# Optimization experiments

Hardware: AMD Instinct MI355X
Metric: run time of the kernel (lower is better)

The kernel has to match this reference:

```python
import jax, jax.numpy as jnp
import numpy as np

GRID_SIZE = 5
SPLINE_ORDER = 3
KH, KW = 3, 3
STRIDE, PAD, DIL = 1, 1, 1


def make_grid(in_features, dtype=jnp.float32):
    # uniform grid over [-1, 1], extended by spline_order on each side
    h = 2.0 / GRID_SIZE
    g = jnp.arange(-SPLINE_ORDER, GRID_SIZE + SPLINE_ORDER + 1, dtype=dtype) * h - 1.0
    return jnp.broadcast_to(g, (in_features, g.shape[0]))  # (in, G)


def b_splines(x, grid):
    # x: (N, in); grid: (in, G). Cox-de Boor recursion.
    xg = x[..., None]  # (N, in, 1)
    bases = ((xg >= grid[:, :-1]) & (xg < grid[:, 1:])).astype(x.dtype)  # (N, in, G-1)
    for k in range(1, SPLINE_ORDER + 1):
        left = (xg - grid[:, : -(k + 1)]) / (grid[:, k:-1] - grid[:, : -(k + 1)])
        right = (grid[:, k + 1:] - xg) / (grid[:, k + 1:] - grid[:, 1:-k])
        bases = left * bases[..., :-1] + right * bases[..., 1:]
    return bases  # (N, in, grid_size + spline_order)


def setup_inputs() -> dict:
    key = jax.random.key(0)
    k1, k2, k3, k4 = jax.random.split(key, 4)
    B, C, H, W = 4, 64, 64, 64
    out_ch = 128
    patch_dim = C * KH * KW  # 576
    nbasis = GRID_SIZE + SPLINE_ORDER  # 8
    x = jax.random.normal(k1, (B, C, H, W), dtype=jnp.float32)
    base_weight = jax.random.normal(k2, (out_ch, patch_dim), dtype=jnp.float32) * 0.05
    spline_weight = jax.random.normal(k3, (out_ch, patch_dim, nbasis), dtype=jnp.float32) * 0.05
    spline_scaler = jax.random.normal(k4, (out_ch, patch_dim), dtype=jnp.float32) * 0.1 + 1.0
    return {"x": x, "base_weight": base_weight, "spline_weight": spline_weight, "spline_scaler": spline_scaler}


def reference(x, base_weight, spline_weight, spline_scaler):
    B, C, H, W = x.shape
    out_ch, patch_dim = base_weight.shape
    # im2col: (B, C*KH*KW, Ho, Wo), feature dim ordered (C, kh, kw) like F.unfold
    patches = jax.lax.conv_general_dilated_patches(
        x, filter_shape=(KH, KW), window_strides=(STRIDE, STRIDE),
        padding=((PAD, PAD), (PAD, PAD)), rhs_dilation=(DIL, DIL),
        dimension_numbers=("NCHW", "OIHW", "NCHW"))
    Ho = (H + 2 * PAD - DIL * (KH - 1) - 1) // STRIDE + 1
    Wo = (W + 2 * PAD - DIL * (KW - 1) - 1) // STRIDE + 1
    L = Ho * Wo
    p = patches.reshape(B, patch_dim, L).transpose(0, 2, 1).reshape(B * L, patch_dim)  # (N, D)
    grid = make_grid(patch_dim, p.dtype)
    base_out = jax.nn.silu(p) @ base_weight.T  # (N, out)
    bases = b_splines(p, grid)  # (N, D, nbasis)
    scaled_w = spline_weight * spline_scaler[..., None]  # (out, D, nbasis)
    spline_out = jnp.einsum("ndk,odk->no", bases, scaled_w)
    out = (base_out + spline_out).reshape(B, L, out_ch).transpose(0, 2, 1).reshape(B, out_ch, Ho, Wo)
    return out
```

## Files before the change

kernel.cpp:

```cpp
#include <hip/hip_runtime.h>
#include <hip/hip_bf16.h>

#define B_      4
#define C_IN    64
#define H_      64
#define W_      64
#define OUT_CH  128
#define HP_     66
#define CF      576
#define WP_BYTES  (9 * OUT_CH * CF * 2)
#define F_BYTES   (B_ * HP_ * HP_ * CF * 2)
#define P_OFFSET  (WP_BYTES + F_BYTES)

typedef __bf16 bf16x8 __attribute__((ext_vector_type(8)));
typedef float  f32x4  __attribute__((ext_vector_type(4)));
typedef _Float16 half8 __attribute__((ext_vector_type(8)));

__device__ __forceinline__ void compute_features(float x, float f[9]) {
    f[0] = x / (1.0f + __expf(-x));
    float g[12];
#pragma unroll
    for (int i = 0; i < 12; ++i) g[i] = (float)(i - 3) * 0.4f - 1.0f;
    float bb[11];
#pragma unroll
    for (int i = 0; i < 11; ++i) bb[i] = (x >= g[i] && x < g[i + 1]) ? 1.0f : 0.0f;
#pragma unroll
    for (int i = 0; i < 10; ++i)
        bb[i] = (x - g[i]) * (1.0f / (g[i + 1] - g[i])) * bb[i]
              + (g[i + 2] - x) * (1.0f / (g[i + 2] - g[i + 1])) * bb[i + 1];
#pragma unroll
    for (int i = 0; i < 9; ++i)
        bb[i] = (x - g[i]) * (1.0f / (g[i + 2] - g[i])) * bb[i]
              + (g[i + 3] - x) * (1.0f / (g[i + 3] - g[i + 1])) * bb[i + 1];
#pragma unroll
    for (int i = 0; i < 8; ++i)
        bb[i] = (x - g[i]) * (1.0f / (g[i + 3] - g[i])) * bb[i]
              + (g[i + 4] - x) * (1.0f / (g[i + 4] - g[i + 1])) * bb[i + 1];
#pragma unroll
    for (int i = 0; i < 8; ++i) f[1 + i] = bb[i];
}

__global__ __launch_bounds__(256) void prep_kernel(
        const float* __restrict__ x, __hip_bfloat16* __restrict__ F,
        const float* __restrict__ bw, const float* __restrict__ sw,
        const float* __restrict__ sc, __hip_bfloat16* __restrict__ Wp) {
    __shared__ float xs[64][33];
    int blk = blockIdx.x;
    int tid = threadIdx.x;

    if (blk >= 528) {
        int idx = (blk - 528) * 256 + tid;
        if (idx < 589824) {
            int o = idx / 4608;
            int r = idx - o * 4608;
            int d = r >> 3;
            int j = r & 7;
            int tap = d % 9;
            int c   = d / 9;
            float v = sw[idx] * sc[o * 576 + d];
            Wp[(tap * OUT_CH + o) * CF + (j + 1) * 64 + c] = __float2bfloat16(v);
        } else {
            int k = idx - 589824;
            int o = k / 576;
            int d = k - o * 576;
            int tap = d % 9;
            int c   = d / 9;
            Wp[(tap * OUT_CH + o) * CF + c] = __float2bfloat16(bw[k]);
        }
        return;
    }

    int half = blk & 1;
    int bh   = blk >> 1;
    int b  = bh / HP_;
    int hp = bh % HP_;
    int h  = hp - 1;

    float f0[9];
    compute_features(0.0f, f0);

    bool interior_row = (h >= 0) && (h < H_);
    if (interior_row) {
        int wl = tid & 31;
        int c8 = tid >> 5;
#pragma unroll
        for (int i = 0; i < 8; ++i) {
            int c = c8 * 8 + i;
            xs[c][wl] = x[((b * C_IN + c) * H_ + h) * W_ + half * 32 + wl];
        }
    }
    __syncthreads();

    int c  = tid & 63;
    int wg = tid >> 6;
    __hip_bfloat16* Frow = F + (size_t)((b * HP_ + hp) * HP_) * CF;

    if (!interior_row) {
        for (int wp = half * 33 + wg; wp < half * 33 + 33; wp += 4) {
            __hip_bfloat16* dst = Frow + (size_t)wp * CF + c;
#pragma unroll
            for (int j = 0; j < 9; ++j) dst[j * 64] = __float2bfloat16(f0[j]);
        }
        return;
    }
    if (half == 0 && wg == 0) {
        __hip_bfloat16* dst = Frow + c;
#pragma unroll
        for (int j = 0; j < 9; ++j) dst[j * 64] = __float2bfloat16(f0[j]);
    }
    if (half == 1 && wg == 3) {
        __hip_bfloat16* dst = Frow + (size_t)65 * CF + c;
#pragma unroll
        for (int j = 0; j < 9; ++j) dst[j * 64] = __float2bfloat16(f0[j]);
    }
    for (int w2l = wg; w2l < 32; w2l += 4) {
        float xv = xs[c][w2l];
        float f[9];
        compute_features(xv, f);
        int wp = half * 32 + w2l + 1;
        __hip_bfloat16* dst = Frow + (size_t)wp * CF + c;
#pragma unroll
        for (int j = 0; j < 9; ++j) dst[j * 64] = __float2bfloat16(f[j]);
    }
}

__global__ __launch_bounds__(256, 2) void gemm_kernel(
        const __hip_bfloat16* __restrict__ Fb, const __hip_bfloat16* __restrict__ Wpb,
        _Float16* __restrict__ P) {
    __shared__ __align__(16) ushort As[2][8192];
    __shared__ __align__(16) ushort Bs[2][8192];

    const ushort* F  = (const ushort*)Fb;
    const ushort* Wp = (const ushort*)Wpb;

    int tid  = threadIdx.x;
    int lane = tid & 63;
    int w    = tid >> 6;
    int l15  = lane & 15;
    int lq   = lane >> 4;
    int wm = w & 1;
    int wn = w >> 1;
    int srow = lane >> 3;
    int sl7  = lane & 7;
    int c8s  = sl7 ^ srow;

    int blk = blockIdx.x;
    int g   = blk >> 7;
    int t   = blk & 127;
    int b   = t >> 5;
    int ho0 = (t & 31) << 1;
    int c0 = (g == 0) ? 0 : (21 + 20 * (g - 1));
    int c1 = c0 + ((g == 0) ? 21 : 20);

    f32x4 acc[4][4];
#pragma unroll
    for (int i = 0; i < 4; ++i)
#pragma unroll
        for (int j = 0; j < 4; ++j) acc[i][j] = (f32x4){0.f, 0.f, 0.f, 0.f};

    auto prefetch = [&](int ch, int buf) {
        int tap = ch / 9;
        int kc  = ch - tap * 9;
        int kh  = tap / 3;
        int kw  = tap - kh * 3;
#pragma unroll
        for (int rr = 0; rr < 4; ++rr) {
            int row = (rr * 4 + w) * 8 + srow;
            int hp = ho0 + (row >> 6) + kh;
            int wp = (row & 63) + kw;
            const ushort* srcA = F + (size_t)((b * HP_ + hp) * HP_ + wp) * CF
                                   + kc * 64 + c8s * 8;
            __builtin_amdgcn_global_load_lds(
                (const __attribute__((address_space(1))) unsigned int*)srcA,
                (__attribute__((address_space(3))) unsigned int*)&As[buf][(rr * 4 + w) * 512],
                16, 0, 0);
            const ushort* srcB = Wp + (size_t)(tap * OUT_CH + row) * CF
                                    + kc * 64 + c8s * 8;
            __builtin_amdgcn_global_load_lds(
                (const __attribute__((address_space(1))) unsigned int*)srcB,
                (__attribute__((address_space(3))) unsigned int*)&Bs[buf][(rr * 4 + w) * 512],
                16, 0, 0);
        }
    };

    int buf = 0;
    prefetch(c0, 0);
    prefetch(c0 + 1, 1);
    for (int ch = c0; ch < c1; ++ch) {
        if (ch + 1 < c1) asm volatile("s_waitcnt vmcnt(8)\n\ts_barrier" ::: "memory");
        else             asm volatile("s_waitcnt vmcnt(0)\n\ts_barrier" ::: "memory");

        bf16x8 af[2][4], bq[2][4];
#pragma unroll
        for (int ks = 0; ks < 2; ++ks) {
#pragma unroll
            for (int mt = 0; mt < 4; ++mt) {
                int o  = wm * 64 + mt * 16 + l15;
                int sl = o * 8 + ((ks * 4 + lq) ^ (o & 7));
                af[ks][mt] = *(const bf16x8*)&Bs[buf][sl * 8];
            }
#pragma unroll
            for (int nt = 0; nt < 4; ++nt) {
                int p  = wn * 64 + nt * 16 + l15;
                int sl = p * 8 + ((ks * 4 + lq) ^ (p & 7));
                bq[ks][nt] = *(const bf16x8*)&As[buf][sl * 8];
            }
        }

        __builtin_amdgcn_s_setprio(1);
#pragma unroll
        for (int ks = 0; ks < 2; ++ks)
#pragma unroll
            for (int mt = 0; mt < 4; ++mt)
#pragma unroll
                for (int nt = 0; nt < 4; ++nt)
                    acc[mt][nt] = __builtin_amdgcn_mfma_f32_16x16x32_bf16(
                        af[ks][mt], bq[ks][nt], acc[mt][nt], 0, 0, 0);
        __builtin_amdgcn_s_setprio(0);

        asm volatile("s_waitcnt lgkmcnt(0)\n\ts_barrier" ::: "memory");
        if (ch + 2 < c1) prefetch(ch + 2, buf);
        buf ^= 1;
    }

    _Float16* Pg = P + ((size_t)(g * 4 + b) * OUT_CH) * 4096 + ho0 * 64;
#pragma unroll
    for (int mt = 0; mt < 4; ++mt) {
        int o = wm * 64 + mt * 16 + lq * 4;
#pragma unroll
        for (int nt = 0; nt < 4; ++nt) {
            int pix = wn * 64 + nt * 16 + l15;
            _Float16* dst = Pg + (size_t)o * 4096 + pix;
#pragma unroll
            for (int rr = 0; rr < 4; ++rr)
                dst[(size_t)rr * 4096] = (_Float16)acc[mt][nt][rr];
        }
    }
}

__global__ __launch_bounds__(256) void reduce_kernel(
        const half8* __restrict__ P, float4* __restrict__ out) {
    const int GS = 262144;
    int i = blockIdx.x * 256 + threadIdx.x;
    half8 a = P[i], bb = P[GS + i], c = P[2 * GS + i], d = P[3 * GS + i];
    float4 o0, o1;
#pragma unroll
    for (int j = 0; j < 4; ++j)
        ((float*)&o0)[j] = (float)a[j] + (float)bb[j] + (float)c[j] + (float)d[j];
#pragma unroll
    for (int j = 0; j < 4; ++j)
        ((float*)&o1)[j] = (float)a[4 + j] + (float)bb[4 + j] + (float)c[4 + j] + (float)d[4 + j];
    out[i * 2]     = o0;
    out[i * 2 + 1] = o1;
}

extern "C" void kernel_launch(void* const* d_in, const int* in_sizes, int n_in,
                              void* d_out, int out_size, void* d_ws, size_t ws_size,
                              hipStream_t stream) {
    const float* x  = (const float*)d_in[0];
    const float* bw = (const float*)d_in[1];
    const float* sw = (const float*)d_in[2];
    const float* sc = (const float*)d_in[3];
    float* out = (float*)d_out;

    __hip_bfloat16* Wp = (__hip_bfloat16*)d_ws;
    __hip_bfloat16* F  = (__hip_bfloat16*)((char*)d_ws + WP_BYTES);
    _Float16*       P  = (_Float16*)((char*)d_ws + P_OFFSET);

    prep_kernel<<<528 + 2592, 256, 0, stream>>>(x, F, bw, sw, sc, Wp);
    gemm_kernel<<<512, 256, 0, stream>>>(F, Wp, P);
    reduce_kernel<<<1024, 256, 0, stream>>>((const half8*)P, (float4*)out);
}
```

Before: 107.3 us.

## Vectorize prep kernel stores and move GEMM prefetch before MFMA loop

The weight-packing branch now has each thread produce eight consecutive output elements and write them with one 16-byte store, gathering the strided inputs. This replaces scattered 2-byte stores and cuts the weight-prep block count from 2592 to 324. Feature generation also packs eight channels per thread into 16-byte stores instead of per-element bf16 writes. In the GEMM, the barrier and the next-chunk prefetch now come right after the LDS fragment reads and before the MFMAs, so global loads overlap with compute. The cost is uncoalesced gather reads in the weight prep.

```diff
diff --git a/kernel.cpp b/kernel.cpp
--- a/kernel.cpp
+++ b/kernel.cpp
@@ -15,6 +15,7 @@
 typedef __bf16 bf16x8 __attribute__((ext_vector_type(8)));
 typedef float  f32x4  __attribute__((ext_vector_type(4)));
 typedef _Float16 half8 __attribute__((ext_vector_type(8)));
+typedef unsigned short ushort8 __attribute__((ext_vector_type(8)));
 
 __device__ __forceinline__ void compute_features(float x, float f[9]) {
     f[0] = x / (1.0f + __expf(-x));
@@ -38,6 +39,11 @@
               + (g[i + 4] - x) * (1.0f / (g[i + 4] - g[i + 1])) * bb[i + 1];
 #pragma unroll
     for (int i = 0; i < 8; ++i) f[1 + i] = bb[i];
+}
+
+__device__ __forceinline__ ushort bf16bits(float v) {
+    __hip_bfloat16 h = __float2bfloat16(v);
+    return *reinterpret_cast<ushort*>(&h);
 }
 
 __global__ __launch_bounds__(256) void prep_kernel(
@@ -49,24 +55,24 @@
     int tid = threadIdx.x;
 
     if (blk >= 528) {
-        int idx = (blk - 528) * 256 + tid;
-        if (idx < 589824) {
-            int o = idx / 4608;
-            int r = idx - o * 4608;
-            int d = r >> 3;
-            int j = r & 7;
-            int tap = d % 9;
-            int c   = d / 9;
-            float v = sw[idx] * sc[o * 576 + d];
-            Wp[(tap * OUT_CH + o) * CF + (j + 1) * 64 + c] = __float2bfloat16(v);
-        } else {
-            int k = idx - 589824;
-            int o = k / 576;
-            int d = k - o * 576;
-            int tap = d % 9;
-            int c   = d / 9;
-            Wp[(tap * OUT_CH + o) * CF + c] = __float2bfloat16(bw[k]);
-        }
+        int widx = ((blk - 528) * 256 + tid) * 8;
+        int tap  = widx / 73728;
+        int rem  = widx - tap * 73728;
+        int o    = rem / 576;
+        int s    = rem - o * 576;
+        int jj   = s >> 6;
+        int c0v  = s & 63;
+        ushort8 v;
+#pragma unroll
+        for (int e = 0; e < 8; ++e) {
+            int c = c0v + e;
+            int d = c * 9 + tap;
+            float val = (jj == 0)
+                ? bw[o * 576 + d]
+                : sw[(o * 576 + d) * 8 + (jj - 1)] * sc[o * 576 + d];
+            v[e] = bf16bits(val);
+        }
+        *(ushort8*)((ushort*)Wp + widx) = v;
         return;
     }
 
@@ -76,52 +82,59 @@
     int hp = bh % HP_;
     int h  = hp - 1;
 
-    float f0[9];
-    compute_features(0.0f, f0);
-
     bool interior_row = (h >= 0) && (h < H_);
     if (interior_row) {
         int wl = tid & 31;
-        int c8 = tid >> 5;
+        int cq = tid >> 5;
 #pragma unroll
         for (int i = 0; i < 8; ++i) {
-            int c = c8 * 8 + i;
+            int c = cq * 8 + i;
             xs[c][wl] = x[((b * C_IN + c) * H_ + h) * W_ + half * 32 + wl];
         }
     }
     __syncthreads();
 
-    int c  = tid & 63;
-    int wg = tid >> 6;
-    __hip_bfloat16* Frow = F + (size_t)((b * HP_ + hp) * HP_) * CF;
+    int w2 = tid >> 3;
+    int c8 = tid & 7;
+    ushort* Frow = (ushort*)F + (size_t)((b * HP_ + hp) * HP_) * CF;
+
+    float f0[9];
+    compute_features(0.0f, f0);
+    ushort8 v0[9];
+#pragma unroll
+    for (int j = 0; j < 9; ++j) {
+        ushort bits = bf16bits(f0[j]);
+#pragma unroll
+        for (int i = 0; i < 8; ++i) v0[j][i] = bits;
+    }
 
     if (!interior_row) {
-        for (int wp = half * 33 + wg; wp < half * 33 + 33; wp += 4) {
-            __hip_bfloat16* dst = Frow + (size_t)wp * CF + c;
-#pragma unroll
-            for (int j = 0; j < 9; ++j) dst[j * 64] = __float2bfloat16(f0[j]);
+        for (int wp = half * 33 + w2; wp < half * 33 + 33; wp += 32) {
+            ushort* dst = Frow + (size_t)wp * CF + c8 * 8;
+#pragma unroll
+            for (int j = 0; j < 9; ++j) *(ushort8*)(dst + j * 64) = v0[j];
         }
         return;
     }
-    if (half == 0 && wg == 0) {
-        __hip_bfloat16* dst = Frow + c;
-#pragma unroll
-        for (int j = 0; j < 9; ++j) dst[j * 64] = __float2bfloat16(f0[j]);
-    }
-    if (half == 1 && wg == 3) {
-        __hip_bfloat16* dst = Frow + (size_t)65 * CF + c;
-#pragma unroll
-        for (int j = 0; j < 9; ++j) dst[j * 64] = __float2bfloat16(f0[j]);
-    }
-    for (int w2l = wg; w2l < 32; w2l += 4) {
-        float xv = xs[c][w2l];
+    if (w2 == 0) {
+        int wph = half ? 65 : 0;
+        ushort* dst = Frow + (size_t)wph * CF + c8 * 8;
+#pragma unroll
+        for (int j = 0; j < 9; ++j) *(ushort8*)(dst + j * 64) = v0[j];
+    }
+    ushort8 v[9];
+#pragma unroll
+    for (int i = 0; i < 8; ++i) {
+        float xv = xs[c8 * 8 + i][w2];
         float f[9];
         compute_features(xv, f);
-        int wp = half * 32 + w2l + 1;
-        __hip_bfloat16* dst = Frow + (size_t)wp * CF + c;
-#pragma unroll
-        for (int j = 0; j < 9; ++j) dst[j * 64] = __float2bfloat16(f[j]);
-    }
+#pragma unroll
+        for (int j = 0; j < 9; ++j) v[j][i] = bf16bits(f[j]);
+    }
+    int wp = half * 32 + w2 + 1;
+    ushort* dst = Frow + (size_t)wp * CF + c8 * 8;
+#pragma unroll
+    for (int j = 0; j < 9; ++j) *(ushort8*)(dst + j * 64) = v[j];
 }
 
 __global__ __launch_bounds__(256, 2) void gemm_kernel(
@@ -206,6 +219,8 @@
                 bq[ks][nt] = *(const bf16x8*)&As[buf][sl * 8];
             }
         }
+        asm volatile("s_waitcnt lgkmcnt(0)\n\ts_barrier" ::: "memory");
+        if (ch + 2 < c1) prefetch(ch + 2, buf);
 
         __builtin_amdgcn_s_setprio(1);
 #pragma unroll
@@ -217,9 +232,6 @@
                     acc[mt][nt] = __builtin_amdgcn_mfma_f32_16x16x32_bf16(
                         af[ks][mt], bq[ks][nt], acc[mt][nt], 0, 0, 0);
         __builtin_amdgcn_s_setprio(0);
-
-        asm volatile("s_waitcnt lgkmcnt(0)\n\ts_barrier" ::: "memory");
-        if (ch + 2 < c1) prefetch(ch + 2, buf);
         buf ^= 1;
     }
 
@@ -267,7 +279,7 @@
     __hip_bfloat16* F  = (__hip_bfloat16*)((char*)d_ws + WP_BYTES);
     _Float16*       P  = (_Float16*)((char*)d_ws + P_OFFSET);
 
-    prep_kernel<<<528 + 2592, 256, 0, stream>>>(x, F, bw, sw, sc, Wp);
+    prep_kernel<<<528 + 324, 256, 0, stream>>>(x, F, bw, sw, sc, Wp);
     gemm_kernel<<<512, 256, 0, stream>>>(F, Wp, P);
     reduce_kernel<<<1024, 256, 0, stream>>>((const half8*)P, (float4*)out);
 }
```

Result: faster. 101.8 us (median of 2 runs) (-5.1%).
